# Kernel optimization log

Measured on AMD Instinct MI355X. Metric: run time of the kernel, lower is better.

Reference implementation:

```python
import jax, jax.numpy as jnp
import numpy as np
from jax import lax

L = 41                                  # filter_length
H = 32                                  # hidden_size
XVALS = jnp.arange((-L) // 2, L // 2, dtype=jnp.float32)  # [-21, ..., 19], length 41 (matches torch.arange(-41//2, 41//2))


def _gauss_bank(mu, sig, C):
    # mu, sig, C: [H] -> filter bank [H, L]
    return C[:, None] * jnp.exp(-0.5 * ((XVALS[None, :] - mu[:, None]) / sig[:, None]) ** 2)


def _depthwise(z, filt):
    # z: [T, H], filt: [H, L] -> VALID cross-correlation per channel, [T-L+1, H]
    out = lax.conv_general_dilated(
        z.T[None],                      # [1, H, T] (NCH)
        filt[:, None, :],               # [H, 1, L] (OIH)
        window_strides=(1,), padding='VALID',
        feature_group_count=z.shape[1])
    return out[0].T


def setup_inputs() -> dict:
    key = jax.random.key(0)
    ks = jax.random.split(key, 8)
    T, D = 262144, 256
    x0 = jax.random.normal(ks[0], (T, 128), jnp.float32)
    x1 = jax.random.normal(ks[1], (T, 128), jnp.float32)
    W1 = jax.random.normal(ks[2], (H, D), jnp.float32) * 0.1   # fc1.weight [hidden, input]
    b1 = jax.random.normal(ks[3], (H,), jnp.float32) * 0.1     # fc1.bias
    V2 = jax.random.normal(ks[4], (D, H), jnp.float32)         # raw fc2 weight (Sphere-parametrized)
    b2 = jax.random.normal(ks[5], (D,), jnp.float32) * 0.1     # fc2.bias
    mus = jax.random.normal(ks[6], (2, H), jnp.float32) * 3.0
    sigmas = 1.0 + 2.0 * jax.random.uniform(ks[7], (2, H), jnp.float32)
    scaling = jnp.ones((2, H), jnp.float32)
    return {"x0": x0, "x1": x1, "W1": W1, "b1": b1, "V2": V2,
            "b2": b2, "mus": mus, "sigmas": sigmas, "scaling": scaling}


def reference(x0, x1, W1, b1, V2, b2, mus, sigmas, scaling):
    # Clamp (straight-through in bwd; forward value is clamp(min=1))
    std = jnp.clip(sigmas, 1.0, None)
    d = x0.shape[1]

    # ---- encode: per-region projection then per-channel Gaussian (flipped-mu) filters
    z0 = x0 @ W1[:, :d].T               # [T, H]
    z1 = x1 @ W1[:, d:].T               # [T, H]
    z = (_depthwise(z0, _gauss_bank(-mus[0], std[0], scaling[0]))
         + _depthwise(z1, _gauss_bank(-mus[1], std[1], scaling[1]))
         + b1)                          # [T-L+1, H]

    # ---- decode: Sphere-normalized readout (unit-norm columns of V2)
    W2 = V2 / jnp.linalg.norm(V2, axis=0, keepdims=True)  # [D, H]
    zd0 = _depthwise(z, _gauss_bank(mus[0], std[0], scaling[0]))  # [T-2L+2, H]
    zd1 = _depthwise(z, _gauss_bank(mus[1], std[1], scaling[1]))
    xh0 = zd0 @ W2[:d].T + b2[:d]       # [T-2L+2, d]
    xh1 = zd1 @ W2[d:].T + b2[d:]
    # model is untrained -> returns (zs dict, x_hats dict); flattened as tuple
    return (zd0, zd1, xh0, xh1)
```

## Files before the change

kernel.cpp:

```cpp
#include <hip/hip_runtime.h>
#include <math.h>

#define FL 41
#define NH 32
#define WS_E0  0
#define WS_E1  1312
#define WS_G0  2624
#define WS_G1  3936
#define WS_W2T 5248

__global__ __launch_bounds__(256) void setup_kernel(
    const float* __restrict__ V2, const float* __restrict__ mus,
    const float* __restrict__ sigmas, const float* __restrict__ scaling,
    float* __restrict__ ws)
{
    const int tid = threadIdx.x;
    __shared__ float nrm[NH];
    {
        const int h = tid >> 3;
        const int s = tid & 7;
        float p = 0.f;
        for (int jj = 0; jj < 32; ++jj) {
            const float v = V2[(s + jj*8)*NH + h];
            p += v*v;
        }
        p += __shfl_xor(p, 1, 8);
        p += __shfl_xor(p, 2, 8);
        p += __shfl_xor(p, 4, 8);
        if (s == 0) nrm[h] = sqrtf(p);
    }
    __syncthreads();
    for (int idx = tid; idx < NH*256; idx += 256) {
        int h = idx >> 8, j = idx & 255;
        ws[WS_W2T + idx] = V2[j*NH + h] / nrm[h];
    }
    for (int idx = tid; idx < 4*NH*FL; idx += 256) {
        int bank = idx / (NH*FL);
        int rem  = idx - bank*(NH*FL);
        int h = rem / FL, l = rem - h*FL;
        int r = bank & 1;
        float mu = mus[r*NH + h];
        float sg = fmaxf(sigmas[r*NH + h], 1.0f);
        float C  = scaling[r*NH + h];
        float m  = (bank < 2) ? -mu : mu;
        float x  = (float)(l - 21);
        float dd = (x - m) / sg;
        ws[idx] = C * expf(-0.5f * dd * dd);
    }
}

__global__ __launch_bounds__(256) void proj_kernel(
    const float* __restrict__ x0, const float* __restrict__ x1,
    const float* __restrict__ W1,
    float* __restrict__ z0, float* __restrict__ z1, int T)
{
    __shared__ float xT[2][32][132];
    __shared__ float wT[2][32][36];
    const int tid  = threadIdx.x;
    const int row0 = blockIdx.x * 128;

    const int reg = tid >> 7;
    const int h0  = ((tid >> 5) & 3) * 8;
    const int m   = tid & 31;

    float acc[4][8];
#pragma unroll
    for (int i = 0; i < 4; ++i)
#pragma unroll
        for (int j = 0; j < 8; ++j) acc[i][j] = 0.f;

    for (int kc = 0; kc < 4; ++kc) {
        const int c0 = kc * 32;
#pragma unroll
        for (int r = 0; r < 2; ++r) {
            const float* __restrict__ xp = r ? x1 : x0;
#pragma unroll
            for (int p = 0; p < 4; ++p) {
                const int row = p*32 + (tid >> 3);
                const int c   = (tid & 7) * 4;
                const float4 v = *reinterpret_cast<const float4*>(
                    &xp[(size_t)(row0 + row)*128 + c0 + c]);
                xT[r][c+0][row] = v.x; xT[r][c+1][row] = v.y;
                xT[r][c+2][row] = v.z; xT[r][c+3][row] = v.w;
            }
        }
        {
            const int h = tid >> 3;
            const int c = (tid & 7) * 4;
            const float4 a = *reinterpret_cast<const float4*>(&W1[h*256 + c0 + c]);
            wT[0][c+0][h] = a.x; wT[0][c+1][h] = a.y;
            wT[0][c+2][h] = a.z; wT[0][c+3][h] = a.w;
            const float4 b = *reinterpret_cast<const float4*>(&W1[h*256 + 128 + c0 + c]);
            wT[1][c+0][h] = b.x; wT[1][c+1][h] = b.y;
            wT[1][c+2][h] = b.z; wT[1][c+3][h] = b.w;
        }
        __syncthreads();
#pragma unroll
        for (int c = 0; c < 32; ++c) {
            const float4 xv = *reinterpret_cast<const float4*>(&xT[reg][c][m*4]);
            const float4 wa = *reinterpret_cast<const float4*>(&wT[reg][c][h0]);
            const float4 wb = *reinterpret_cast<const float4*>(&wT[reg][c][h0+4]);
            const float xs[4] = {xv.x, xv.y, xv.z, xv.w};
            const float wv[8] = {wa.x, wa.y, wa.z, wa.w, wb.x, wb.y, wb.z, wb.w};
#pragma unroll
            for (int i = 0; i < 4; ++i)
#pragma unroll
                for (int j = 0; j < 8; ++j) acc[i][j] += xs[i] * wv[j];
        }
        __syncthreads();
    }
    float* __restrict__ zp = reg ? z1 : z0;
#pragma unroll
    for (int i = 0; i < 4; ++i) {
        const size_t r = (size_t)(row0 + m*4 + i) * NH + h0;
        float4 o0 = make_float4(acc[i][0], acc[i][1], acc[i][2], acc[i][3]);
        float4 o1 = make_float4(acc[i][4], acc[i][5], acc[i][6], acc[i][7]);
        *reinterpret_cast<float4*>(&zp[r])   = o0;
        *reinterpret_cast<float4*>(&zp[r+4]) = o1;
    }
}

__global__ __launch_bounds__(256) void encode_kernel(
    const float* __restrict__ z0, const float* __restrict__ z1,
    const float* __restrict__ b1, const float* __restrict__ ws,
    float* __restrict__ z, int T, int T1)
{
    __shared__ float s0[104][NH];
    __shared__ float s1[104][NH];
    const int tid = threadIdx.x;
    const int t0  = blockIdx.x * 64;
    for (int idx = tid; idx < 104*NH/4; idx += 256) {
        const int f = idx*4, row = f >> 5, col = f & 31;
        const int gr = t0 + row;
        if (gr < T) {
            *reinterpret_cast<float4*>(&s0[row][col]) =
                *reinterpret_cast<const float4*>(&z0[(size_t)gr*NH + col]);
            *reinterpret_cast<float4*>(&s1[row][col]) =
                *reinterpret_cast<const float4*>(&z1[(size_t)gr*NH + col]);
        }
    }
    __syncthreads();
    const int h = tid & 31;
    const int g = tid >> 5;
    float e0r[FL], e1r[FL];
#pragma unroll
    for (int l = 0; l < FL; ++l) {
        e0r[l] = ws[WS_E0 + h*FL + l];
        e1r[l] = ws[WS_E1 + h*FL + l];
    }
    float acc[8];
    const float bb = b1[h];
#pragma unroll
    for (int i = 0; i < 8; ++i) acc[i] = bb;
    const int tb = g * 8;
#pragma unroll
    for (int s = 0; s < 48; ++s) {
        const float a0 = s0[tb + s][h];
        const float a1 = s1[tb + s][h];
#pragma unroll
        for (int i = 0; i < 8; ++i) {
            const int l = s - i;
            if (l >= 0 && l < FL) acc[i] += a0*e0r[l] + a1*e1r[l];
        }
    }
#pragma unroll
    for (int i = 0; i < 8; ++i) {
        const int t = t0 + tb + i;
        if (t < T1) z[(size_t)t*NH + h] = acc[i];
    }
}

__global__ __launch_bounds__(256) void decode_kernel(
    const float* __restrict__ z, const float* __restrict__ ws,
    float* __restrict__ zd0, float* __restrict__ zd1, int T1, int T2)
{
    __shared__ float sz[72][NH];
    const int tid = threadIdx.x;
    const int t0  = blockIdx.x * 32;
    for (int idx = tid; idx < 72*NH/4; idx += 256) {
        const int f = idx*4, row = f >> 5, col = f & 31;
        const int gr = t0 + row;
        if (gr < T1)
            *reinterpret_cast<float4*>(&sz[row][col]) =
                *reinterpret_cast<const float4*>(&z[(size_t)gr*NH + col]);
    }
    __syncthreads();
    const int h = tid & 31;
    const int r = (tid >> 5) & 1;
    const int g = tid >> 6;
    float fr[FL];
    const float* __restrict__ fb = ws + (r ? WS_G1 : WS_G0);
#pragma unroll
    for (int l = 0; l < FL; ++l) fr[l] = fb[h*FL + l];
    float acc[8];
#pragma unroll
    for (int i = 0; i < 8; ++i) acc[i] = 0.f;
    const int tb = g * 8;
#pragma unroll
    for (int s = 0; s < 48; ++s) {
        const float a = sz[tb + s][h];
#pragma unroll
        for (int i = 0; i < 8; ++i) {
            const int l = s - i;
            if (l >= 0 && l < FL) acc[i] += a * fr[l];
        }
    }
    float* __restrict__ zd = r ? zd1 : zd0;
#pragma unroll
    for (int i = 0; i < 8; ++i) {
        const int t = t0 + tb + i;
        if (t < T2) zd[(size_t)t*NH + h] = acc[i];
    }
}

__global__ __launch_bounds__(256) void readout_kernel(
    const float* __restrict__ zd0, const float* __restrict__ zd1,
    const float* __restrict__ W2T, const float* __restrict__ b2,
    float* __restrict__ xh0, float* __restrict__ xh1, int T2)
{
    __shared__ float w2[NH][260];
    __shared__ float zT[2][NH][34];
    const int tid = threadIdx.x;
    const int t0  = blockIdx.x * 32;

    for (int idx = tid; idx < NH*256/4; idx += 256) {
        const int f = idx*4, h = f >> 8, j = f & 255;
        *reinterpret_cast<float4*>(&w2[h][j]) =
            *reinterpret_cast<const float4*>(&W2T[h*256 + j]);
    }
    for (int idx = tid; idx < 512; idx += 256) {
        const int r   = idx >> 8;
        const int rem = idx & 255;
        const int tl  = rem >> 3;
        const int hh  = (rem & 7) * 4;
        const int t   = t0 + tl;
        float4 v = make_float4(0.f, 0.f, 0.f, 0.f);
        if (t < T2) {
            const float* __restrict__ zp = r ? zd1 : zd0;
            v = *reinterpret_cast<const float4*>(&zp[(size_t)t*NH + hh]);
        }
        zT[r][hh+0][tl] = v.x; zT[r][hh+1][tl] = v.y;
        zT[r][hh+2][tl] = v.z; zT[r][hh+3][tl] = v.w;
    }
    __syncthreads();

    const int m  = tid & 15;
    const int jq = tid >> 4;
    const int jb = jq * 4;

    float acc[2][16];
#pragma unroll
    for (int k = 0; k < 4; ++k)
#pragma unroll
        for (int c = 0; c < 4; ++c) {
            const float bv = b2[jb + 64*k + c];
            acc[0][4*k+c] = bv;
            acc[1][4*k+c] = bv;
        }

#pragma unroll 4
    for (int h = 0; h < NH; ++h) {
        const float2 za = *reinterpret_cast<const float2*>(&zT[0][h][m*2]);
        const float2 zb = *reinterpret_cast<const float2*>(&zT[1][h][m*2]);
        const float4 w0 = *reinterpret_cast<const float4*>(&w2[h][jb]);
        const float4 w1 = *reinterpret_cast<const float4*>(&w2[h][jb + 64]);
        const float4 w2v= *reinterpret_cast<const float4*>(&w2[h][jb + 128]);
        const float4 w3 = *reinterpret_cast<const float4*>(&w2[h][jb + 192]);
        acc[0][0]  += za.x*w0.x; acc[0][1]  += za.x*w0.y;
        acc[0][2]  += za.x*w0.z; acc[0][3]  += za.x*w0.w;
        acc[0][4]  += za.x*w1.x; acc[0][5]  += za.x*w1.y;
        acc[0][6]  += za.x*w1.z; acc[0][7]  += za.x*w1.w;
        acc[0][8]  += zb.x*w2v.x; acc[0][9]  += zb.x*w2v.y;
        acc[0][10] += zb.x*w2v.z; acc[0][11] += zb.x*w2v.w;
        acc[0][12] += zb.x*w3.x; acc[0][13] += zb.x*w3.y;
        acc[0][14] += zb.x*w3.z; acc[0][15] += zb.x*w3.w;
        acc[1][0]  += za.y*w0.x; acc[1][1]  += za.y*w0.y;
        acc[1][2]  += za.y*w0.z; acc[1][3]  += za.y*w0.w;
        acc[1][4]  += za.y*w1.x; acc[1][5]  += za.y*w1.y;
        acc[1][6]  += za.y*w1.z; acc[1][7]  += za.y*w1.w;
        acc[1][8]  += zb.y*w2v.x; acc[1][9]  += zb.y*w2v.y;
        acc[1][10] += zb.y*w2v.z; acc[1][11] += zb.y*w2v.w;
        acc[1][12] += zb.y*w3.x; acc[1][13] += zb.y*w3.y;
        acc[1][14] += zb.y*w3.z; acc[1][15] += zb.y*w3.w;
    }

#pragma unroll
    for (int i = 0; i < 2; ++i) {
        const int t = t0 + m*2 + i;
        if (t < T2) {
#pragma unroll
            for (int k = 0; k < 4; ++k) {
                float* __restrict__ xp = (k < 2) ? xh0 : xh1;
                const int jl = jb + 64 * (k & 1);
                float4 o = make_float4(acc[i][4*k+0], acc[i][4*k+1],
                                       acc[i][4*k+2], acc[i][4*k+3]);
                *reinterpret_cast<float4*>(&xp[(size_t)t*128 + jl]) = o;
            }
        }
    }
}

extern "C" void kernel_launch(void* const* d_in, const int* in_sizes, int n_in,
                              void* d_out, int out_size, void* d_ws, size_t ws_size,
                              hipStream_t stream)
{
    const float* x0      = (const float*)d_in[0];
    const float* x1      = (const float*)d_in[1];
    const float* W1      = (const float*)d_in[2];
    const float* b1      = (const float*)d_in[3];
    const float* V2      = (const float*)d_in[4];
    const float* b2      = (const float*)d_in[5];
    const float* mus     = (const float*)d_in[6];
    const float* sigmas  = (const float*)d_in[7];
    const float* scaling = (const float*)d_in[8];
    float* out = (float*)d_out;
    float* ws  = (float*)d_ws;

    const int T  = in_sizes[0] / 128;
    const int T1 = T - 40;
    const int T2 = T - 80;

    float* zd0 = out;
    float* zd1 = out + (size_t)T2 * NH;
    float* xh0 = out + (size_t)2 * T2 * NH;
    float* xh1 = xh0 + (size_t)T2 * 128;

    float* z0 = xh0;
    float* z1 = xh0 + (size_t)T * NH;
    float* z  = xh1;

    setup_kernel<<<1, 256, 0, stream>>>(V2, mus, sigmas, scaling, ws);
    proj_kernel<<<T / 128, 256, 0, stream>>>(x0, x1, W1, z0, z1, T);
    encode_kernel<<<(T1 + 63) / 64, 256, 0, stream>>>(z0, z1, b1, ws, z, T, T1);
    decode_kernel<<<(T2 + 31) / 32, 256, 0, stream>>>(z, ws, zd0, zd1, T1, T2);
    readout_kernel<<<(T2 + 31) / 32, 256, 0, stream>>>(zd0, zd1, ws + WS_W2T, b2,
                                                       xh0, xh1, T2);
}
```

Baseline: 674.8 us.

## Fuse encode and decode convolutions into one kernel with shared-memory intermediate

Merges the encode and decode depthwise convolutions into a single 512-thread kernel. The intermediate z tile (176 rows including halo) stays in shared memory instead of going through a global write and re-read. This costs recomputing about 48 halo rows per 128-row block and more LDS per block. The readout kernel is also widened to 512 threads and 64 rows per block.

Result: faster. 658.6 us (-2.4%).

```diff
diff --git a/kernel.cpp b/kernel.cpp
--- a/kernel.cpp
+++ b/kernel.cpp
@@ -120,117 +120,118 @@
     }
 }
 
-__global__ __launch_bounds__(256) void encode_kernel(
+#define ED_BT 128
+#define ED_RS 216
+#define ED_ZR 176
+__global__ __launch_bounds__(512) void encdec_kernel(
     const float* __restrict__ z0, const float* __restrict__ z1,
     const float* __restrict__ b1, const float* __restrict__ ws,
-    float* __restrict__ z, int T, int T1)
-{
-    __shared__ float s0[104][NH];
-    __shared__ float s1[104][NH];
+    float* __restrict__ zd0, float* __restrict__ zd1,
+    int T, int T2)
+{
+    __shared__ float s0[ED_RS][NH];
+    __shared__ float s1[ED_RS][NH];
+    __shared__ float zt[ED_ZR][NH];
     const int tid = threadIdx.x;
-    const int t0  = blockIdx.x * 64;
-    for (int idx = tid; idx < 104*NH/4; idx += 256) {
+    const int t0  = blockIdx.x * ED_BT;
+
+    for (int idx = tid; idx < ED_RS*NH/4; idx += 512) {
         const int f = idx*4, row = f >> 5, col = f & 31;
         const int gr = t0 + row;
+        float4 a = make_float4(0.f,0.f,0.f,0.f);
+        float4 b = make_float4(0.f,0.f,0.f,0.f);
         if (gr < T) {
-            *reinterpret_cast<float4*>(&s0[row][col]) =
-                *reinterpret_cast<const float4*>(&z0[(size_t)gr*NH + col]);
-            *reinterpret_cast<float4*>(&s1[row][col]) =
-                *reinterpret_cast<const float4*>(&z1[(size_t)gr*NH + col]);
-        }
+            a = *reinterpret_cast<const float4*>(&z0[(size_t)gr*NH + col]);
+            b = *reinterpret_cast<const float4*>(&z1[(size_t)gr*NH + col]);
+        }
+        *reinterpret_cast<float4*>(&s0[row][col]) = a;
+        *reinterpret_cast<float4*>(&s1[row][col]) = b;
     }
     __syncthreads();
+
     const int h = tid & 31;
-    const int g = tid >> 5;
-    float e0r[FL], e1r[FL];
-#pragma unroll
-    for (int l = 0; l < FL; ++l) {
-        e0r[l] = ws[WS_E0 + h*FL + l];
-        e1r[l] = ws[WS_E1 + h*FL + l];
-    }
-    float acc[8];
-    const float bb = b1[h];
-#pragma unroll
-    for (int i = 0; i < 8; ++i) acc[i] = bb;
-    const int tb = g * 8;
-#pragma unroll
-    for (int s = 0; s < 48; ++s) {
-        const float a0 = s0[tb + s][h];
-        const float a1 = s1[tb + s][h];
-#pragma unroll
-        for (int i = 0; i < 8; ++i) {
-            const int l = s - i;
-            if (l >= 0 && l < FL) acc[i] += a0*e0r[l] + a1*e1r[l];
-        }
-    }
-#pragma unroll
-    for (int i = 0; i < 8; ++i) {
-        const int t = t0 + tb + i;
-        if (t < T1) z[(size_t)t*NH + h] = acc[i];
-    }
-}
-
-__global__ __launch_bounds__(256) void decode_kernel(
-    const float* __restrict__ z, const float* __restrict__ ws,
-    float* __restrict__ zd0, float* __restrict__ zd1, int T1, int T2)
-{
-    __shared__ float sz[72][NH];
-    const int tid = threadIdx.x;
-    const int t0  = blockIdx.x * 32;
-    for (int idx = tid; idx < 72*NH/4; idx += 256) {
-        const int f = idx*4, row = f >> 5, col = f & 31;
-        const int gr = t0 + row;
-        if (gr < T1)
-            *reinterpret_cast<float4*>(&sz[row][col]) =
-                *reinterpret_cast<const float4*>(&z[(size_t)gr*NH + col]);
+    {
+        const int g  = tid >> 5;
+        const int tb = g * 11;
+        float acc[11];
+        const float bb = b1[h];
+#pragma unroll
+        for (int i = 0; i < 11; ++i) acc[i] = bb;
+        float fr[FL];
+#pragma unroll
+        for (int l = 0; l < FL; ++l) fr[l] = ws[WS_E0 + h*FL + l];
+#pragma unroll
+        for (int s = 0; s < 51; ++s) {
+            const float a0 = s0[tb + s][h];
+#pragma unroll
+            for (int i = 0; i < 11; ++i) {
+                const int l = s - i;
+                if (l >= 0 && l < FL) acc[i] += a0 * fr[l];
+            }
+        }
+#pragma unroll
+        for (int l = 0; l < FL; ++l) fr[l] = ws[WS_E1 + h*FL + l];
+#pragma unroll
+        for (int s = 0; s < 51; ++s) {
+            const float a1 = s1[tb + s][h];
+#pragma unroll
+            for (int i = 0; i < 11; ++i) {
+                const int l = s - i;
+                if (l >= 0 && l < FL) acc[i] += a1 * fr[l];
+            }
+        }
+#pragma unroll
+        for (int i = 0; i < 11; ++i) zt[tb + i][h] = acc[i];
     }
     __syncthreads();
-    const int h = tid & 31;
-    const int r = (tid >> 5) & 1;
-    const int g = tid >> 6;
-    float fr[FL];
-    const float* __restrict__ fb = ws + (r ? WS_G1 : WS_G0);
-#pragma unroll
-    for (int l = 0; l < FL; ++l) fr[l] = fb[h*FL + l];
-    float acc[8];
-#pragma unroll
-    for (int i = 0; i < 8; ++i) acc[i] = 0.f;
-    const int tb = g * 8;
-#pragma unroll
-    for (int s = 0; s < 48; ++s) {
-        const float a = sz[tb + s][h];
-#pragma unroll
-        for (int i = 0; i < 8; ++i) {
-            const int l = s - i;
-            if (l >= 0 && l < FL) acc[i] += a * fr[l];
-        }
-    }
-    float* __restrict__ zd = r ? zd1 : zd0;
-#pragma unroll
-    for (int i = 0; i < 8; ++i) {
-        const int t = t0 + tb + i;
-        if (t < T2) zd[(size_t)t*NH + h] = acc[i];
-    }
-}
-
-__global__ __launch_bounds__(256) void readout_kernel(
+
+    {
+        const int rr = (tid >> 5) & 1;
+        const int g  = tid >> 6;
+        const int tb = g * 16;
+        float fr[FL];
+        const float* __restrict__ fb = ws + (rr ? WS_G1 : WS_G0);
+#pragma unroll
+        for (int l = 0; l < FL; ++l) fr[l] = fb[h*FL + l];
+        float acc[16];
+#pragma unroll
+        for (int i = 0; i < 16; ++i) acc[i] = 0.f;
+#pragma unroll
+        for (int s = 0; s < 56; ++s) {
+            const float a = zt[tb + s][h];
+#pragma unroll
+            for (int i = 0; i < 16; ++i) {
+                const int l = s - i;
+                if (l >= 0 && l < FL) acc[i] += a * fr[l];
+            }
+        }
+        float* __restrict__ zd = rr ? zd1 : zd0;
+#pragma unroll
+        for (int i = 0; i < 16; ++i) {
+            const int t = t0 + tb + i;
+            if (t < T2) zd[(size_t)t*NH + h] = acc[i];
+        }
+    }
+}
+
+__global__ __launch_bounds__(512) void readout_kernel(
     const float* __restrict__ zd0, const float* __restrict__ zd1,
     const float* __restrict__ W2T, const float* __restrict__ b2,
     float* __restrict__ xh0, float* __restrict__ xh1, int T2)
 {
     __shared__ float w2[NH][260];
-    __shared__ float zT[2][NH][34];
+    __shared__ float zT[2][NH][66];
     const int tid = threadIdx.x;
-    const int t0  = blockIdx.x * 32;
-
-    for (int idx = tid; idx < NH*256/4; idx += 256) {
-        const int f = idx*4, h = f >> 8, j = f & 255;
+    const int t0  = blockIdx.x * 64;
+
+    for (int idx = tid; idx < 2048; idx += 512) {
+        const int h = idx >> 6, j = (idx & 63) * 4;
         *reinterpret_cast<float4*>(&w2[h][j]) =
             *reinterpret_cast<const float4*>(&W2T[h*256 + j]);
     }
-    for (int idx = tid; idx < 512; idx += 256) {
-        const int r   = idx >> 8;
-        const int rem = idx & 255;
+    for (int idx = tid; idx < 1024; idx += 512) {
+        const int r   = idx >> 9;
+        const int rem = idx & 511;
         const int tl  = rem >> 3;
         const int hh  = (rem & 7) * 4;
         const int t   = t0 + tl;
@@ -244,8 +245,8 @@
     }
     __syncthreads();
 
-    const int m  = tid & 15;
-    const int jq = tid >> 4;
+    const int m  = tid & 31;
+    const int jq = tid >> 5;
     const int jb = jq * 4;
 
     float acc[2][16];
@@ -317,7 +318,6 @@
     float* ws  = (float*)d_ws;
 
     const int T  = in_sizes[0] / 128;
-    const int T1 = T - 40;
     const int T2 = T - 80;
 
     float* zd0 = out;
@@ -327,12 +327,11 @@
 
     float* z0 = xh0;
     float* z1 = xh0 + (size_t)T * NH;
-    float* z  = xh1;
 
     setup_kernel<<<1, 256, 0, stream>>>(V2, mus, sigmas, scaling, ws);
     proj_kernel<<<T / 128, 256, 0, stream>>>(x0, x1, W1, z0, z1, T);
-    encode_kernel<<<(T1 + 63) / 64, 256, 0, stream>>>(z0, z1, b1, ws, z, T, T1);
-    decode_kernel<<<(T2 + 31) / 32, 256, 0, stream>>>(z, ws, zd0, zd1, T1, T2);
-    readout_kernel<<<(T2 + 31) / 32, 256, 0, stream>>>(zd0, zd1, ws + WS_W2T, b2,
+    encdec_kernel<<<(T2 + ED_BT - 1) / ED_BT, 512, 0, stream>>>(
+        z0, z1, b1, ws, zd0, zd1, T, T2);
+    readout_kernel<<<(T2 + 63) / 64, 512, 0, stream>>>(zd0, zd1, ws + WS_W2T, b2,
                                                        xh0, xh1, T2);
 }
```
